# Performance work log

Hardware: AMD Instinct MI355X
Metric: run time of the kernel (lower is better)

Reference implementation:

```python
import jax, jax.numpy as jnp
import numpy as np

HEADS = 8
DIM_HEAD = 64
INNER = HEADS * DIM_HEAD  # 512
DIM = 256
MSA_H = 128  # number of MSA rows
MSA_W = 256  # sequence length


def setup_inputs() -> dict:
    key = jax.random.key(0)
    ks = jax.random.split(key, 8)
    n = MSA_H * MSA_W
    w_std = 0.02
    return {
        "x": jax.random.normal(ks[0], (1, n, DIM), dtype=jnp.float32),
        "wq_w": jax.random.normal(ks[1], (DIM, INNER), dtype=jnp.float32) * w_std,
        "wkv_w": jax.random.normal(ks[2], (DIM, 2 * INNER), dtype=jnp.float32) * w_std,
        "wout_w": jax.random.normal(ks[3], (INNER, DIM), dtype=jnp.float32) * w_std,
        "wout_b": jnp.zeros((DIM,), dtype=jnp.float32),
        "hq_w": jax.random.normal(ks[4], (DIM, INNER), dtype=jnp.float32) * w_std,
        "hkv_w": jax.random.normal(ks[5], (DIM, 2 * INNER), dtype=jnp.float32) * w_std,
        "hout_w": jax.random.normal(ks[6], (INNER, DIM), dtype=jnp.float32) * w_std,
        "hout_b": jnp.zeros((DIM,), dtype=jnp.float32),
        "msa_h": MSA_H,
        "msa_w": MSA_W,
    }


def reference(x, wq_w, wkv_w, wout_w, wout_b, hq_w, hkv_w, hout_w, hout_b, msa_h, msa_w):
    b, n, d = x.shape
    h, w = msa_h, msa_w
    scale = DIM_HEAD ** -0.5
    x4 = x.reshape(b, h, w, d)  # (b, rows, cols, dim)

    # ---- width attention: attend across MSA rows (h), independent per column (w) ----
    xw = jnp.swapaxes(x4, 1, 2)  # (b, w, h, d)
    q = (xw @ wq_w).reshape(b, w, h, HEADS, DIM_HEAD)
    kv = (xw @ wkv_w).reshape(b, w, h, 2, HEADS, DIM_HEAD)
    k, v = kv[..., 0, :, :], kv[..., 1, :, :]
    dots = jnp.einsum('bwiHd,bwjHd->bwHij', q, k) * scale  # (b, w, H, h, h)
    attn = jax.nn.softmax(dots, axis=-1)
    o = jnp.einsum('bwHij,bwjHd->bwiHd', attn, v).reshape(b, w, h, INNER)
    w_out = o @ wout_w + wout_b  # (b, w, h, d)
    w_out = jnp.swapaxes(w_out, 1, 2)  # (b, h, w, d)

    # ---- height attention: attend across columns (w), rows tied (tie_attn_dim = h) ----
    q = (x4 @ hq_w).reshape(b, h, w, HEADS, DIM_HEAD)
    kv = (x4 @ hkv_w).reshape(b, h, w, 2, HEADS, DIM_HEAD)
    k, v = kv[..., 0, :, :], kv[..., 1, :, :]
    tie_scale = scale * (h ** -0.5)
    # scores summed over tied row dim r: 'b r h i d, b r h j d -> b h i j'
    dots = jnp.einsum('briHd,brjHd->bHij', q, k) * tie_scale  # (b, H, w, w)
    attn = jax.nn.softmax(dots, axis=-1)
    o = jnp.einsum('bHij,brjHd->briHd', attn, v).reshape(b, h, w, INNER)
    h_out = o @ hout_w + hout_b  # (b, h, w, d)

    out = w_out + h_out
    return out.reshape(b, h * w, d)
```

## Files before the change

### kernel.cpp

```cpp
#include <hip/hip_runtime.h>

typedef short s16x8 __attribute__((ext_vector_type(8)));
typedef float f32x4 __attribute__((ext_vector_type(4)));

#define MFMA16(a, b, c) __builtin_amdgcn_mfma_f32_16x16x32_bf16((a), (b), (c), 0, 0, 0)

__device__ __forceinline__ unsigned short f2b(float f) {
  union { float f; unsigned int u; } v; v.f = f;
  unsigned int u = v.u;
  unsigned int r = (u + 0x7fffu + ((u >> 16) & 1u)) >> 16;
  return (unsigned short)r;
}
__device__ __forceinline__ float b2f(unsigned short b) {
  union { unsigned int u; float f; } v; v.u = ((unsigned int)b) << 16;
  return v.f;
}

__device__ __forceinline__ void gld_lds16(const void* g, void* l) {
  __builtin_amdgcn_global_load_lds(
      (const __attribute__((address_space(1))) unsigned int*)g,
      (__attribute__((address_space(3))) unsigned int*)l, 16, 0, 0);
}

__global__ __launch_bounds__(256) void cvt_x(const float* __restrict__ x,
                                             unsigned short* __restrict__ xb) {
  size_t i = ((size_t)blockIdx.x * 256 + threadIdx.x) * 4;
  float4 v = *(const float4*)(x + i);
  ushort4 o;
  o.x = f2b(v.x); o.y = f2b(v.y); o.z = f2b(v.z); o.w = f2b(v.w);
  *(ushort4*)(xb + i) = o;
}

__global__ __launch_bounds__(256) void build_wt(const float* __restrict__ wq,
                                                const float* __restrict__ wkv,
                                                const float* __restrict__ hq,
                                                const float* __restrict__ hkv,
                                                unsigned short* __restrict__ WT) {
  const int n = blockIdx.x, k = threadIdx.x;
  float v;
  if (n < 512)       v = wq [(size_t)k * 512  + n];
  else if (n < 1536) v = wkv[(size_t)k * 1024 + (n - 512)];
  else if (n < 2048) v = hq [(size_t)k * 512  + (n - 1536)];
  else               v = hkv[(size_t)k * 1024 + (n - 2048)];
  WT[(size_t)n * 256 + k] = f2b(v);
}

__global__ __launch_bounds__(256) void build_w2t(const float* __restrict__ wout,
                                                 const float* __restrict__ hout,
                                                 unsigned short* __restrict__ W2T) {
  const int n = blockIdx.x;
  for (int k = threadIdx.x; k < 1024; k += 256) {
    const float v = (k < 512) ? wout[(size_t)k * 256 + n] : hout[(size_t)(k - 512) * 256 + n];
    W2T[(size_t)n * 1024 + k] = f2b(v);
  }
}

__global__ __launch_bounds__(512) void gemm_qkv(const unsigned short* __restrict__ X,
                                                const unsigned short* __restrict__ WT,
                                                unsigned short* __restrict__ C,
                                                int branch) {
  __shared__ unsigned short As[128 * 32];
  __shared__ unsigned short Bs[128 * 32];
  const int tid = threadIdx.x, wave = tid >> 6, lane = tid & 63;
  const int q = lane >> 4, l = lane & 15;
  const int xcd = blockIdx.x & 7;
  const int c = blockIdx.x >> 3;
  const int m0 = (xcd * 32 + (c & 31)) * 128;
  const int n0 = (c >> 5) * 128;
  const int mt = (wave >> 1) * 32;
  const int nt = (wave & 1) * 64;
  const char* Xb = (const char*)X;
  const char* Wb = (const char*)WT;
  const int srow = tid >> 2;
  const int sboff = (tid & 3) * 16;
  char* AsB = (char*)As;
  char* BsB = (char*)Bs;
  f32x4 acc[2][4] = {};
#pragma unroll
  for (int ks = 0; ks < 8; ++ks) {
    const int kb = ks * 64;
    gld_lds16(Xb + (size_t)(m0 + srow) * 512 + kb + sboff, AsB + tid * 16);
    gld_lds16(Wb + (size_t)(n0 + srow) * 512 + kb + sboff, BsB + tid * 16);
    __syncthreads();
    s16x8 a[2], b[4];
#pragma unroll
    for (int i = 0; i < 2; ++i) a[i] = *(const s16x8*)(&As[(mt + i * 16 + l) * 32 + q * 8]);
#pragma unroll
    for (int j = 0; j < 4; ++j) b[j] = *(const s16x8*)(&Bs[(nt + j * 16 + l) * 32 + q * 8]);
#pragma unroll
    for (int i = 0; i < 2; ++i)
#pragma unroll
      for (int j = 0; j < 4; ++j) acc[i][j] = MFMA16(b[j], a[i], acc[i][j]);
    __syncthreads();
  }
#pragma unroll
  for (int i = 0; i < 2; ++i) {
    const int m = m0 + mt + i * 16 + l;
    const int mrow = (branch == 0) ? ((m & 255) * 8) : ((m >> 8) * 8);
    const int mcol = (branch == 0) ? (m >> 8) : (m & 255);
    const int mdim = (branch == 0) ? 128 : 256;
#pragma unroll
    for (int j = 0; j < 4; ++j) {
      const int n = n0 + nt + j * 16 + q * 4;
      const int part = n >> 9, H = (n & 511) >> 6, d = n & 63;
      ushort4 o;
      o.x = f2b(acc[i][j][0]); o.y = f2b(acc[i][j][1]);
      o.z = f2b(acc[i][j][2]); o.w = f2b(acc[i][j][3]);
      unsigned short* base = C + (size_t)part * 16777216;
      const size_t idx = ((size_t)(mrow + H) * mdim + mcol) * 64 + d;
      *(ushort4*)(base + idx) = o;
    }
  }
}

__global__ __launch_bounds__(256) void col_attn(const unsigned short* __restrict__ C,
                                                unsigned short* __restrict__ O) {
  __shared__ __align__(16) char lds[50176];
  char* QK = lds;
  unsigned short* Vt = (unsigned short*)(lds + 32768);
  const int w = blockIdx.x, H = blockIdx.y;
  const int tid = threadIdx.x, wave = tid >> 6, lane = tid & 63;
  const int q = lane >> 4, l = lane & 15;
  const size_t slab = (size_t)(w * 8 + H) * 8192;
  const unsigned short* Qs = C + slab;
  const unsigned short* Ks = C + 16777216 + slab;
  const unsigned short* Vs = C + 33554432 + slab;
#pragma unroll
  for (int it = 0; it < 8; ++it) {
    const int u = it * 256 + tid;
    const int half = u >> 10;
    const int vv = u & 1023;
    const int r = vv >> 3, ch = vv & 7;
    const char* src = (const char*)(half ? Ks : Qs);
    gld_lds16(src + (size_t)r * 128 + ((ch ^ (r & 7)) * 16), QK + u * 16);
  }
  for (int u = tid; u < 1024; u += 256) {
    const int j = u >> 3, db = u & 7;
    s16x8 v = *(const s16x8*)(Vs + j * 64 + db * 8);
#pragma unroll
    for (int t = 0; t < 8; ++t) Vt[(db * 8 + t) * 136 + j] = v[t];
  }
  __syncthreads();
  const int m0 = wave * 32;
  f32x4 acc[2][8] = {};
#pragma unroll
  for (int ks = 0; ks < 2; ++ks) {
    s16x8 a[2], b[8];
#pragma unroll
    for (int i = 0; i < 2; ++i) {
      const int ra = m0 + i * 16 + l;
      a[i] = *(const s16x8*)(QK + (size_t)ra * 128 + (((ks * 4 + q) ^ (ra & 7)) * 16));
    }
#pragma unroll
    for (int j = 0; j < 8; ++j) {
      const int rb = j * 16 + l;
      b[j] = *(const s16x8*)(QK + 16384 + (size_t)rb * 128 + (((ks * 4 + q) ^ (rb & 7)) * 16));
    }
#pragma unroll
    for (int i = 0; i < 2; ++i)
#pragma unroll
      for (int j = 0; j < 8; ++j) acc[i][j] = MFMA16(a[i], b[j], acc[i][j]);
  }
  __syncthreads();
#pragma unroll
  for (int i = 0; i < 2; ++i)
#pragma unroll
    for (int r = 0; r < 4; ++r) {
      float v[8];
#pragma unroll
      for (int j = 0; j < 8; ++j) v[j] = acc[i][j][r] * 0.125f;
      float mx = fmaxf(fmaxf(fmaxf(v[0], v[1]), fmaxf(v[2], v[3])),
                       fmaxf(fmaxf(v[4], v[5]), fmaxf(v[6], v[7])));
      mx = fmaxf(mx, __shfl_xor(mx, 1));
      mx = fmaxf(mx, __shfl_xor(mx, 2));
      mx = fmaxf(mx, __shfl_xor(mx, 4));
      mx = fmaxf(mx, __shfl_xor(mx, 8));
      float s = 0.f;
#pragma unroll
      for (int j = 0; j < 8; ++j) { v[j] = __expf(v[j] - mx); s += v[j]; }
      s += __shfl_xor(s, 1);
      s += __shfl_xor(s, 2);
      s += __shfl_xor(s, 4);
      s += __shfl_xor(s, 8);
      const float inv = 1.0f / s;
      const int row = m0 + i * 16 + q * 4 + r;
#pragma unroll
      for (int j = 0; j < 8; ++j) {
        const int ch = 2 * j + (l >> 3);
        *(unsigned short*)(QK + (size_t)row * 256 + ((ch ^ (row & 7)) * 16) + (l & 7) * 2) =
            f2b(v[j] * inv);
      }
    }
  f32x4 o[2][4] = {};
#pragma unroll
  for (int ks = 0; ks < 4; ++ks) {
    const int kk = ks * 32 + q * 8;
    s16x8 a[2], b[4];
#pragma unroll
    for (int i = 0; i < 2; ++i) {
      const int ra = m0 + i * 16 + l;
      a[i] = *(const s16x8*)(QK + (size_t)ra * 256 + (((ks * 4 + q) ^ (ra & 7)) * 16));
    }
#pragma unroll
    for (int j = 0; j < 4; ++j) b[j] = *(const s16x8*)(&Vt[(j * 16 + l) * 136 + kk]);
#pragma unroll
    for (int i = 0; i < 2; ++i)
#pragma unroll
      for (int j = 0; j < 4; ++j) o[i][j] = MFMA16(a[i], b[j], o[i][j]);
  }
#pragma unroll
  for (int i = 0; i < 2; ++i)
#pragma unroll
    for (int j = 0; j < 4; ++j)
#pragma unroll
      for (int r = 0; r < 4; ++r) {
        const int row = m0 + i * 16 + q * 4 + r;
        const int d = j * 16 + l;
        O[(size_t)(row * 256 + w) * 1024 + H * 64 + d] = f2b(o[i][j][r]);
      }
}

__global__ __launch_bounds__(256) void row_dots(const unsigned short* __restrict__ C,
                                                float* __restrict__ dp) {
  const int H = blockIdx.z;
  const int r0 = blockIdx.y * 16;
  const int ti = blockIdx.x & 1, tj = blockIdx.x >> 1;
  const int tid = threadIdx.x, wave = tid >> 6, lane = tid & 63;
  const int q = lane >> 4, l = lane & 15;
  const int m0 = ti * 128 + (wave >> 1) * 64;
  const int n0 = tj * 128 + (wave & 1) * 64;
  const unsigned short* Qh = C;
  const unsigned short* Kh = C + 16777216;
  f32x4 acc[4][4] = {};
  for (int ks = 0; ks < 32; ++ks) {
    const int k = ks * 32 + q * 8;
    const int rr = r0 + (k >> 6), d = k & 63;
    const size_t slab = (size_t)(rr * 8 + H) * 16384;
    s16x8 a[4], b[4];
#pragma unroll
    for (int i = 0; i < 4; ++i) a[i] = *(const s16x8*)(Qh + slab + (m0 + i * 16 + l) * 64 + d);
#pragma unroll
    for (int j = 0; j < 4; ++j) b[j] = *(const s16x8*)(Kh + slab + (n0 + j * 16 + l) * 64 + d);
#pragma unroll
    for (int i = 0; i < 4; ++i)
#pragma unroll
      for (int j = 0; j < 4; ++j) acc[i][j] = MFMA16(a[i], b[j], acc[i][j]);
  }
  float* outp = dp + ((size_t)blockIdx.y * 8 + H) * 65536;
#pragma unroll
  for (int i = 0; i < 4; ++i)
#pragma unroll
    for (int j = 0; j < 4; ++j)
#pragma unroll
      for (int r = 0; r < 4; ++r)
        outp[(size_t)(m0 + i * 16 + q * 4 + r) * 256 + n0 + j * 16 + l] = acc[i][j][r];
}

__global__ __launch_bounds__(256) void row_softmax(const float* __restrict__ dp,
                                                   unsigned short* __restrict__ attn) {
  const int row = blockIdx.x;
  const int H = row >> 8, i = row & 255;
  const int t = threadIdx.x, wave = t >> 6, lane = t & 63;
  __shared__ float red[8];
  float v = 0.f;
#pragma unroll
  for (int c = 0; c < 8; ++c) v += dp[((size_t)c * 8 + H) * 65536 + (size_t)i * 256 + t];
  v *= 1.1048543456e-2f;
  float m = v;
  for (int o = 32; o > 0; o >>= 1) m = fmaxf(m, __shfl_xor(m, o, 64));
  if (lane == 0) red[wave] = m;
  __syncthreads();
  const float M = fmaxf(fmaxf(red[0], red[1]), fmaxf(red[2], red[3]));
  const float e = __expf(v - M);
  float s = e;
  for (int o = 32; o > 0; o >>= 1) s += __shfl_xor(s, o, 64);
  if (lane == 0) red[4 + wave] = s;
  __syncthreads();
  const float S = red[4] + red[5] + red[6] + red[7];
  attn[(size_t)row * 256 + t] = f2b(e / S);
}

__global__ __launch_bounds__(256) void row_pv(const unsigned short* __restrict__ C,
                                              const unsigned short* __restrict__ attn,
                                              unsigned short* __restrict__ O) {
  __shared__ unsigned short Vt[64 * 264];
  const int r = blockIdx.x, H = blockIdx.y;
  const int tid = threadIdx.x, wave = tid >> 6, lane = tid & 63;
  const int q = lane >> 4, l = lane & 15;
  const unsigned short* Vs = C + 33554432 + (size_t)(r * 8 + H) * 16384;
  for (int u = tid; u < 2048; u += 256) {
    const int j = u >> 3, db = u & 7;
    s16x8 v = *(const s16x8*)(Vs + j * 64 + db * 8);
#pragma unroll
    for (int t = 0; t < 8; ++t) Vt[(db * 8 + t) * 264 + j] = v[t];
  }
  __syncthreads();
  const unsigned short* A = attn + (size_t)H * 65536;
  const int m0 = wave * 64;
  f32x4 acc[4][4] = {};
#pragma unroll
  for (int ks = 0; ks < 8; ++ks) {
    const int kk = ks * 32 + q * 8;
    s16x8 a[4], b[4];
#pragma unroll
    for (int i = 0; i < 4; ++i) a[i] = *(const s16x8*)(A + (size_t)(m0 + i * 16 + l) * 256 + kk);
#pragma unroll
    for (int j = 0; j < 4; ++j) b[j] = *(const s16x8*)(&Vt[(j * 16 + l) * 264 + kk]);
#pragma unroll
    for (int i = 0; i < 4; ++i)
#pragma unroll
      for (int j = 0; j < 4; ++j) acc[i][j] = MFMA16(a[i], b[j], acc[i][j]);
  }
#pragma unroll
  for (int i = 0; i < 4; ++i)
#pragma unroll
    for (int j = 0; j < 4; ++j)
#pragma unroll
      for (int rr = 0; rr < 4; ++rr) {
        const int iw = m0 + i * 16 + q * 4 + rr;
        const int d = j * 16 + l;
        O[(size_t)(r * 256 + iw) * 1024 + 512 + H * 64 + d] = f2b(acc[i][j][rr]);
      }
}

__global__ __launch_bounds__(256) void out_proj(const unsigned short* __restrict__ O,
                                                const unsigned short* __restrict__ W2T,
                                                const float* __restrict__ bw,
                                                const float* __restrict__ bh,
                                                float* __restrict__ out) {
  __shared__ unsigned short As[128 * 32];
  __shared__ unsigned short Bs[128 * 32];
  const int tid = threadIdx.x, wave = tid >> 6, lane = tid & 63;
  const int q = lane >> 4, l = lane & 15;
  const int m0 = blockIdx.x * 128;
  const int n0 = blockIdx.y * 128;
  const int mt = (wave >> 1) * 64;
  const int nt = (wave & 1) * 64;
  const char* Ob = (const char*)O;
  const char* Wb = (const char*)W2T;
  const int srow = wave * 32 + (lane >> 2);
  const int sboff = (lane & 3) * 16;
  char* AsB = (char*)As;
  char* BsB = (char*)Bs;
  f32x4 acc[4][4] = {};
  for (int ks = 0; ks < 32; ++ks) {
    const int kb = ks * 64;
    gld_lds16(Ob + (size_t)(m0 + srow) * 2048 + kb + sboff, AsB + wave * 2048);
    gld_lds16(Ob + (size_t)(m0 + srow + 16) * 2048 + kb + sboff, AsB + wave * 2048 + 1024);
    gld_lds16(Wb + (size_t)(n0 + srow) * 2048 + kb + sboff, BsB + wave * 2048);
    gld_lds16(Wb + (size_t)(n0 + srow + 16) * 2048 + kb + sboff, BsB + wave * 2048 + 1024);
    __syncthreads();
    s16x8 a[4], b[4];
#pragma unroll
    for (int i = 0; i < 4; ++i) a[i] = *(const s16x8*)(&As[(mt + i * 16 + l) * 32 + q * 8]);
#pragma unroll
    for (int j = 0; j < 4; ++j) b[j] = *(const s16x8*)(&Bs[(nt + j * 16 + l) * 32 + q * 8]);
#pragma unroll
    for (int i = 0; i < 4; ++i)
#pragma unroll
      for (int j = 0; j < 4; ++j) acc[i][j] = MFMA16(a[i], b[j], acc[i][j]);
    __syncthreads();
  }
#pragma unroll
  for (int i = 0; i < 4; ++i)
#pragma unroll
    for (int j = 0; j < 4; ++j) {
      const int col = n0 + nt + j * 16 + l;
      const float bias = bw[col] + bh[col];
#pragma unroll
      for (int r = 0; r < 4; ++r)
        out[(size_t)(m0 + mt + i * 16 + q * 4 + r) * 256 + col] = acc[i][j][r] + bias;
    }
}

extern "C" void kernel_launch(void* const* d_in, const int* in_sizes, int n_in,
                              void* d_out, int out_size, void* d_ws, size_t ws_size,
                              hipStream_t stream) {
  const float* x    = (const float*)d_in[0];
  const float* wq   = (const float*)d_in[1];
  const float* wkv  = (const float*)d_in[2];
  const float* wout = (const float*)d_in[3];
  const float* bw   = (const float*)d_in[4];
  const float* hq   = (const float*)d_in[5];
  const float* hkv  = (const float*)d_in[6];
  const float* hout = (const float*)d_in[7];
  const float* bh   = (const float*)d_in[8];
  float* out = (float*)d_out;

  char* ws = (char*)d_ws;
  unsigned short* x_bf  = (unsigned short*)(ws);
  unsigned short* WcatT = (unsigned short*)(ws + 16777216);
  unsigned short* W2T   = (unsigned short*)(ws + 18350080);
  float*          dp    = (float*)(ws + 18874368);
  unsigned short* attn  = (unsigned short*)(ws + 35651584);
  unsigned short* Ocat  = (unsigned short*)(ws + 36700160);
  unsigned short* Cproj = (unsigned short*)(ws + 103809024);

  cvt_x<<<8192, 256, 0, stream>>>(x, x_bf);
  build_wt<<<3072, 256, 0, stream>>>(wq, wkv, hq, hkv, WcatT);
  build_w2t<<<256, 256, 0, stream>>>(wout, hout, W2T);

  gemm_qkv<<<3072, 512, 0, stream>>>(x_bf, WcatT, Cproj, 0);
  col_attn<<<dim3(256, 8), 256, 0, stream>>>(Cproj, Ocat);
  gemm_qkv<<<3072, 512, 0, stream>>>(x_bf, WcatT + 1536 * 256, Cproj, 1);
  row_dots<<<dim3(4, 8, 8), 256, 0, stream>>>(Cproj, dp);
  row_softmax<<<2048, 256, 0, stream>>>(dp, attn);
  row_pv<<<dim3(128, 8), 256, 0, stream>>>(Cproj, attn, Ocat);
  out_proj<<<dim3(256, 2), 256, 0, stream>>>(Ocat, W2T, bw, bh, out);
}
```

Baseline: 350.2 us.

## Merge both QKV projection GEMMs into one launch and XCD-swizzle out_proj

Replaces the two per-branch QKV projection launches with a single 6144-block GEMM that writes the width and height branch outputs into separate workspace buffers. It is used only when the workspace is large enough, otherwise the old path runs. This removes one launch and lets the whole projection fill the GPU at once, at the cost of an extra ~100MB workspace buffer. The out_proj grid is also flattened and remapped so that contiguous M tiles land on the same XCD, for better L2 locality.

```diff
diff --git a/kernel.cpp b/kernel.cpp
--- a/kernel.cpp
+++ b/kernel.cpp
@@ -52,6 +52,65 @@
   for (int k = threadIdx.x; k < 1024; k += 256) {
     const float v = (k < 512) ? wout[(size_t)k * 256 + n] : hout[(size_t)(k - 512) * 256 + n];
     W2T[(size_t)n * 1024 + k] = f2b(v);
+  }
+}
+
+__global__ __launch_bounds__(512) void gemm_qkv2(const unsigned short* __restrict__ X,
+                                                 const unsigned short* __restrict__ WT,
+                                                 unsigned short* __restrict__ C0,
+                                                 unsigned short* __restrict__ C1) {
+  __shared__ unsigned short As[128 * 32];
+  __shared__ unsigned short Bs[128 * 32];
+  const int tid = threadIdx.x, wave = tid >> 6, lane = tid & 63;
+  const int q = lane >> 4, l = lane & 15;
+  const int xcd = blockIdx.x & 7;
+  const int c = blockIdx.x >> 3;
+  const int m0 = (xcd * 32 + (c & 31)) * 128;
+  const int n0 = (c >> 5) * 128;
+  const int mt = (wave >> 1) * 32;
+  const int nt = (wave & 1) * 64;
+  const char* Xb = (const char*)X;
+  const char* Wb = (const char*)WT;
+  const int srow = tid >> 2;
+  const int sboff = (tid & 3) * 16;
+  char* AsB = (char*)As;
+  char* BsB = (char*)Bs;
+  f32x4 acc[2][4] = {};
+#pragma unroll
+  for (int ks = 0; ks < 8; ++ks) {
+    const int kb = ks * 64;
+    gld_lds16(Xb + (size_t)(m0 + srow) * 512 + kb + sboff, AsB + tid * 16);
+    gld_lds16(Wb + (size_t)(n0 + srow) * 512 + kb + sboff, BsB + tid * 16);
+    __syncthreads();
+    s16x8 a[2], b[4];
+#pragma unroll
+    for (int i = 0; i < 2; ++i) a[i] = *(const s16x8*)(&As[(mt + i * 16 + l) * 32 + q * 8]);
+#pragma unroll
+    for (int j = 0; j < 4; ++j) b[j] = *(const s16x8*)(&Bs[(nt + j * 16 + l) * 32 + q * 8]);
+#pragma unroll
+    for (int i = 0; i < 2; ++i)
+#pragma unroll
+      for (int j = 0; j < 4; ++j) acc[i][j] = MFMA16(b[j], a[i], acc[i][j]);
+    __syncthreads();
+  }
+  const int br = (n0 >= 1536);
+#pragma unroll
+  for (int i = 0; i < 2; ++i) {
+    const int m = m0 + mt + i * 16 + l;
+    const int mrow = (br == 0) ? ((m & 255) * 8) : ((m >> 8) * 8);
+    const int mcol = (br == 0) ? (m >> 8) : (m & 255);
+    const int mdim = (br == 0) ? 128 : 256;
+#pragma unroll
+    for (int j = 0; j < 4; ++j) {
+      const int nn = n0 + nt + j * 16 + q * 4 - br * 1536;
+      const int part = nn >> 9, H = (nn & 511) >> 6, d = nn & 63;
+      ushort4 o;
+      o.x = f2b(acc[i][j][0]); o.y = f2b(acc[i][j][1]);
+      o.z = f2b(acc[i][j][2]); o.w = f2b(acc[i][j][3]);
+      unsigned short* base = (br ? C1 : C0) + (size_t)part * 16777216;
+      const size_t idx = ((size_t)(mrow + H) * mdim + mcol) * 64 + d;
+      *(ushort4*)(base + idx) = o;
+    }
   }
 }
 
@@ -332,8 +391,10 @@
   __shared__ unsigned short Bs[128 * 32];
   const int tid = threadIdx.x, wave = tid >> 6, lane = tid & 63;
   const int q = lane >> 4, l = lane & 15;
-  const int m0 = blockIdx.x * 128;
-  const int n0 = blockIdx.y * 128;
+  const int xcd = blockIdx.x & 7;
+  const int c = blockIdx.x >> 3;
+  const int m0 = (xcd * 32 + (c >> 1)) * 128;
+  const int n0 = (c & 1) * 128;
   const int mt = (wave >> 1) * 64;
   const int nt = (wave & 1) * 64;
   const char* Ob = (const char*)O;
@@ -394,17 +455,27 @@
   float*          dp    = (float*)(ws + 18874368);
   unsigned short* attn  = (unsigned short*)(ws + 35651584);
   unsigned short* Ocat  = (unsigned short*)(ws + 36700160);
-  unsigned short* Cproj = (unsigned short*)(ws + 103809024);
+  unsigned short* Cproj0 = (unsigned short*)(ws + 103809024);
+  unsigned short* Cproj1 = (unsigned short*)(ws + 103809024 + 100663296);
+  const size_t need2 = 103809024 + 2ull * 100663296;
 
   cvt_x<<<8192, 256, 0, stream>>>(x, x_bf);
   build_wt<<<3072, 256, 0, stream>>>(wq, wkv, hq, hkv, WcatT);
   build_w2t<<<256, 256, 0, stream>>>(wout, hout, W2T);
 
-  gemm_qkv<<<3072, 512, 0, stream>>>(x_bf, WcatT, Cproj, 0);
-  col_attn<<<dim3(256, 8), 256, 0, stream>>>(Cproj, Ocat);
-  gemm_qkv<<<3072, 512, 0, stream>>>(x_bf, WcatT + 1536 * 256, Cproj, 1);
-  row_dots<<<dim3(4, 8, 8), 256, 0, stream>>>(Cproj, dp);
-  row_softmax<<<2048, 256, 0, stream>>>(dp, attn);
-  row_pv<<<dim3(128, 8), 256, 0, stream>>>(Cproj, attn, Ocat);
-  out_proj<<<dim3(256, 2), 256, 0, stream>>>(Ocat, W2T, bw, bh, out);
-}
+  if (ws_size >= need2) {
+    gemm_qkv2<<<6144, 512, 0, stream>>>(x_bf, WcatT, Cproj0, Cproj1);
+    col_attn<<<dim3(256, 8), 256, 0, stream>>>(Cproj0, Ocat);
+    row_dots<<<dim3(4, 8, 8), 256, 0, stream>>>(Cproj1, dp);
+    row_softmax<<<2048, 256, 0, stream>>>(dp, attn);
+    row_pv<<<dim3(128, 8), 256, 0, stream>>>(Cproj1, attn, Ocat);
+  } else {
+    gemm_qkv<<<3072, 512, 0, stream>>>(x_bf, WcatT, Cproj0, 0);
+    col_attn<<<dim3(256, 8), 256, 0, stream>>>(Cproj0, Ocat);
+    gemm_qkv<<<3072, 512, 0, stream>>>(x_bf, WcatT + 1536 * 256, Cproj0, 1);
+    row_dots<<<dim3(4, 8, 8), 256, 0, stream>>>(Cproj0, dp);
+    row_softmax<<<2048, 256, 0, stream>>>(dp, attn);
+    row_pv<<<dim3(128, 8), 256, 0, stream>>>(Cproj0, attn, Ocat);
+  }
+  out_proj<<<512, 256, 0, stream>>>(Ocat, W2T, bw, bh, out);
+}
```

Measured after the change: 352.3 us. Within noise of the previous version (+0.6%).

## Pipeline QKV GEMM global-to-LDS loads with a 4-stage ring buffer

Applied to the files above, without the earlier changes.

Replaces the single-buffered K loop in gemm_qkv with a 4-deep LDS ring buffer, issuing four async global_load_lds stages ahead and waiting on vmcnt counters before each compute step. The aim is to overlap global memory latency with MFMA work instead of fully serializing load and compute at each of the eight K steps. It quadruples LDS usage per block (64 KB), which may reduce occupancy. Correctness depends on the manual vmcnt accounting matching the issued loads.

```diff
diff --git a/kernel.cpp b/kernel.cpp
--- a/kernel.cpp
+++ b/kernel.cpp
@@ -59,8 +59,8 @@
                                                 const unsigned short* __restrict__ WT,
                                                 unsigned short* __restrict__ C,
                                                 int branch) {
-  __shared__ unsigned short As[128 * 32];
-  __shared__ unsigned short Bs[128 * 32];
+  __shared__ unsigned short As[4][128 * 32];
+  __shared__ unsigned short Bs[4][128 * 32];
   const int tid = threadIdx.x, wave = tid >> 6, lane = tid & 63;
   const int q = lane >> 4, l = lane & 15;
   const int xcd = blockIdx.x & 7;
@@ -73,26 +73,49 @@
   const char* Wb = (const char*)WT;
   const int srow = tid >> 2;
   const int sboff = (tid & 3) * 16;
-  char* AsB = (char*)As;
-  char* BsB = (char*)Bs;
   f32x4 acc[2][4] = {};
-#pragma unroll
-  for (int ks = 0; ks < 8; ++ks) {
-    const int kb = ks * 64;
-    gld_lds16(Xb + (size_t)(m0 + srow) * 512 + kb + sboff, AsB + tid * 16);
-    gld_lds16(Wb + (size_t)(n0 + srow) * 512 + kb + sboff, BsB + tid * 16);
-    __syncthreads();
-    s16x8 a[2], b[4];
-#pragma unroll
-    for (int i = 0; i < 2; ++i) a[i] = *(const s16x8*)(&As[(mt + i * 16 + l) * 32 + q * 8]);
-#pragma unroll
-    for (int j = 0; j < 4; ++j) b[j] = *(const s16x8*)(&Bs[(nt + j * 16 + l) * 32 + q * 8]);
-#pragma unroll
-    for (int i = 0; i < 2; ++i)
-#pragma unroll
-      for (int j = 0; j < 4; ++j) acc[i][j] = MFMA16(b[j], a[i], acc[i][j]);
-    __syncthreads();
-  }
+
+#define QKV_STAGE(ks)                                                              \
+  {                                                                                \
+    const int kb_ = (ks) * 64;                                                     \
+    gld_lds16(Xb + (size_t)(m0 + srow) * 512 + kb_ + sboff,                        \
+              (char*)As[(ks) & 3] + tid * 16);                                     \
+    gld_lds16(Wb + (size_t)(n0 + srow) * 512 + kb_ + sboff,                        \
+              (char*)Bs[(ks) & 3] + tid * 16);                                     \
+  }
+
+#define QKV_STEP(ks, VM)                                                           \
+  {                                                                                \
+    asm volatile("s_waitcnt vmcnt(" #VM ")" ::: "memory");                         \
+    __builtin_amdgcn_s_barrier();                                                  \
+    __builtin_amdgcn_sched_barrier(0);                                             \
+    s16x8 a[2], b[4];                                                              \
+    _Pragma("unroll") for (int i = 0; i < 2; ++i)                                  \
+        a[i] = *(const s16x8*)(&As[(ks) & 3][(mt + i * 16 + l) * 32 + q * 8]);     \
+    _Pragma("unroll") for (int j = 0; j < 4; ++j)                                  \
+        b[j] = *(const s16x8*)(&Bs[(ks) & 3][(nt + j * 16 + l) * 32 + q * 8]);     \
+    _Pragma("unroll") for (int i = 0; i < 2; ++i)                                  \
+        _Pragma("unroll") for (int j = 0; j < 4; ++j)                              \
+            acc[i][j] = MFMA16(b[j], a[i], acc[i][j]);           \
+    __builtin_amdgcn_s_barrier();                                                  \
+    asm volatile("" ::: "memory");          \
+  }
+
+  QKV_STAGE(0);
+  QKV_STAGE(1);
+  QKV_STAGE(2);
+  QKV_STAGE(3);
+  QKV_STEP(0, 6) QKV_STAGE(4);
+  QKV_STEP(1, 6) QKV_STAGE(5);
+  QKV_STEP(2, 6) QKV_STAGE(6);
+  QKV_STEP(3, 6) QKV_STAGE(7);
+  QKV_STEP(4, 6);
+  QKV_STEP(5, 4);
+  QKV_STEP(6, 2);
+  QKV_STEP(7, 0);
+#undef QKV_STAGE
+#undef QKV_STEP
+
 #pragma unroll
   for (int i = 0; i < 2; ++i) {
     const int m = m0 + mt + i * 16 + l;
```

Result: no change. 348.8 us (-0.4%).
